# Kernel optimization log

Measured on AMD Instinct MI355X. Metric: run time of the kernel, lower is better.

The kernel has to match this reference:

```python
import jax, jax.numpy as jnp
import numpy as np

EPS = 1e-5
NUM_HEADS = 4


def setup_inputs() -> dict:
    key = jax.random.key(0)
    ks = jax.random.split(key, 6)
    B, C, H, W = 16, 256, 32, 32
    x = jax.random.normal(ks[0], (B, C, H, W), dtype=jnp.float32)
    gamma = jnp.ones((C,), jnp.float32)
    beta = jnp.zeros((C,), jnp.float32)
    run_mean = jax.random.normal(ks[1], (C,), dtype=jnp.float32) * 0.1
    run_var = jax.random.uniform(ks[2], (C,), dtype=jnp.float32, minval=0.5, maxval=1.5)
    qkv_w = jax.random.normal(ks[3], (3 * C, C), dtype=jnp.float32) * (1.0 / np.sqrt(C))
    qkv_b = jnp.zeros((3 * C,), jnp.float32)
    out_w = jax.random.normal(ks[4], (C, C), dtype=jnp.float32) * (1.0 / np.sqrt(C))
    out_b = jnp.zeros((C,), jnp.float32)
    return {"x": x, "gamma": gamma, "beta": beta, "run_mean": run_mean,
            "run_var": run_var, "qkv_w": qkv_w, "qkv_b": qkv_b,
            "out_w": out_w, "out_b": out_b}


def reference(x, gamma, beta, run_mean, run_var, qkv_w, qkv_b, out_w, out_b):
    B, C, H, W = x.shape
    n = NUM_HEADS
    hd = C // n
    # BatchNorm2d (eval mode, running stats)
    inv = jax.lax.rsqrt(run_var + EPS)
    xn = (x - run_mean[:, None, None]) * (inv * gamma)[:, None, None] + beta[:, None, None]
    # 1x1 conv -> QKV: [B, 3C, H, W]
    qkv = jnp.einsum('oc,bchw->bohw', qkv_w, xn) + qkv_b[:, None, None]
    qkv = qkv.reshape(B, n, 3 * hd, H, W)
    q, k, v = qkv[:, :, :hd], qkv[:, :, hd:2 * hd], qkv[:, :, 2 * hd:]
    # full spatial attention; note scale is sqrt(C), per source
    attn = jnp.einsum('bnchw,bncyx->bnhwyx', q, k) / jnp.sqrt(jnp.float32(C))
    attn = jax.nn.softmax(attn.reshape(B, n, H, W, H * W), axis=-1)
    attn = attn.reshape(B, n, H, W, H, W)
    av = jnp.einsum('bnhwyx,bncyx->bnchw', attn, v).reshape(B, C, H, W)
    out = jnp.einsum('oc,bchw->bohw', out_w, av) + out_b[:, None, None]
    return x + out
```

## Files before the change

### kernel.cpp

```cpp
#include <hip/hip_runtime.h>
#include <hip/hip_bf16.h>

__device__ __forceinline__ float bf2f(unsigned short u) {
    return __uint_as_float(((unsigned int)u) << 16);
}
__device__ __forceinline__ unsigned short f2bf(float f) {
    unsigned int u = __float_as_uint(f);
    unsigned int r = (u + 0x7fffu + ((u >> 16) & 1u)) >> 16;
    return (unsigned short)r;
}
__device__ __forceinline__ float ld1(const void* p, long i, bool isf32) {
    return isf32 ? ((const float*)p)[i] : bf2f(((const unsigned short*)p)[i]);
}

typedef __attribute__((ext_vector_type(8))) short bh8;
typedef __attribute__((ext_vector_type(4))) float f32x4;

#define S_TOK 1024
#define C_DIM 256
#define O_QKV 768
#define HD    64
#define NREG  196608
#define QOFF  0
#define KOFF  65536
#define VOFF  131072

__global__ __launch_bounds__(256) void prep_kernel(
    const void* __restrict__ gamma, const void* __restrict__ beta,
    const void* __restrict__ rmean, const void* __restrict__ rvar,
    const void* __restrict__ qkv_w, const void* __restrict__ qkv_b,
    const void* __restrict__ out_w, const void* __restrict__ out_b,
    unsigned short* __restrict__ w1b, float* __restrict__ b1,
    unsigned short* __restrict__ w2b, float* __restrict__ b2, int* __restrict__ flg)
{
    const unsigned g0 = *(const unsigned*)gamma;
    const bool isf32 = (g0 == 0x3F800000u);
    const int c = threadIdx.x;
    const int blk = blockIdx.x;
    if (blk == 0 && c == 0) flg[0] = isf32 ? 1 : 0;
    if (blk < O_QKV) {
        const int o = blk;
        const float v  = ld1(rvar, c, isf32);
        const float a  = ld1(gamma, c, isf32) * rsqrtf(fmaxf(v, 0.f) + 1e-5f);
        const float sh = ld1(beta, c, isf32) - ld1(rmean, c, isf32) * a;
        const float w  = ld1(qkv_w, (long)o * C_DIM + c, isf32);
        w1b[(size_t)o * C_DIM + c] = f2bf(w * a);
        __shared__ float red[256];
        red[c] = w * sh;
        __syncthreads();
        for (int st = 128; st > 0; st >>= 1) {
            if (c < st) red[c] += red[c + st];
            __syncthreads();
        }
        if (c == 0) b1[o] = ld1(qkv_b, o, isf32) + red[0];
    } else {
        const int o = blk - O_QKV;
        w2b[(size_t)o * C_DIM + c] = f2bf(ld1(out_w, (long)o * C_DIM + c, isf32));
        if (c == 0) b2[o] = ld1(out_b, o, isf32);
    }
}

__global__ __launch_bounds__(256) void gemm_qkv_kernel(
    const unsigned short* __restrict__ w1b, const float* __restrict__ b1,
    const void* __restrict__ x, unsigned short* __restrict__ qkv, int b0,
    const int* __restrict__ flg)
{
    const bool isf32 = (flg[0] != 0);
    const int s0 = blockIdx.x * 64;
    const int og = blockIdx.y;
    const int z  = blockIdx.z;
    const int b  = b0 + z;
    const int t  = threadIdx.x;
    const int wave = t >> 6, lane = t & 63;
    const int quad = lane >> 4, l16 = lane & 15;

    __shared__ unsigned short xs[64 * 258];

    const int tok = lane;
#pragma unroll
    for (int it = 0; it < 16; ++it) {
        const int c = (it * 4 + wave) * 4;
        ushort4 w;
        if (isf32) {
            const float* xp = (const float*)x + ((size_t)b * C_DIM + c) * S_TOK + s0 + tok;
            w.x = f2bf(xp[0]);
            w.y = f2bf(xp[S_TOK]);
            w.z = f2bf(xp[2 * S_TOK]);
            w.w = f2bf(xp[3 * S_TOK]);
        } else {
            const unsigned short* xp =
                (const unsigned short*)x + ((size_t)b * C_DIM + c) * S_TOK + s0 + tok;
            w.x = xp[0]; w.y = xp[S_TOK]; w.z = xp[2 * S_TOK]; w.w = xp[3 * S_TOK];
        }
        *(ushort4*)&xs[tok * 258 + c] = w;
    }
    __syncthreads();

    for (int ot = 0; ot < 4; ++ot) {
        const int o0 = og * 256 + ot * 64;
        const int ow = o0 + wave * 16 + l16;
        bh8 af[8];
#pragma unroll
        for (int kc = 0; kc < 8; ++kc)
            af[kc] = *(const bh8*)&w1b[(size_t)ow * C_DIM + kc * 32 + quad * 8];
        f32x4 acc[4];
#pragma unroll
        for (int nt = 0; nt < 4; ++nt) acc[nt] = (f32x4){0.f, 0.f, 0.f, 0.f};
#pragma unroll
        for (int kc = 0; kc < 8; ++kc) {
#pragma unroll
            for (int nt = 0; nt < 4; ++nt) {
                const bh8 bf = *(const bh8*)&xs[(nt * 16 + l16) * 258 + kc * 32 + quad * 8];
                acc[nt] = __builtin_amdgcn_mfma_f32_16x16x32_bf16(af[kc], bf, acc[nt], 0, 0, 0);
            }
        }
        const int n      = o0 / 192;
        const int region = (o0 >> 6) % 3;
        const int och    = wave * 16 + quad * 4;
        float bias_r[4];
#pragma unroll
        for (int r = 0; r < 4; ++r) bias_r[r] = b1[o0 + och + r];
        unsigned short* hb = qkv + (size_t)z * O_QKV * S_TOK + n * NREG;
        if (region < 2) {
            const float sc = (region == 0) ? 0.0625f : 1.0f;
            unsigned short* qb = hb + (region == 0 ? QOFF : KOFF);
#pragma unroll
            for (int nt = 0; nt < 4; ++nt) {
                const int tk = s0 + nt * 16 + l16;
                ushort4 rr;
                rr.x = f2bf((acc[nt][0] + bias_r[0]) * sc);
                rr.y = f2bf((acc[nt][1] + bias_r[1]) * sc);
                rr.z = f2bf((acc[nt][2] + bias_r[2]) * sc);
                rr.w = f2bf((acc[nt][3] + bias_r[3]) * sc);
                *(ushort4*)&qb[(size_t)tk * 64 + och] = rr;
            }
        } else {
            unsigned short* vb = hb + VOFF;
#pragma unroll
            for (int nt = 0; nt < 4; ++nt) {
                const int tk = s0 + nt * 16 + l16;
#pragma unroll
                for (int r = 0; r < 4; ++r)
                    vb[(size_t)(och + r) * S_TOK + tk] = f2bf(acc[nt][r] + bias_r[r]);
            }
        }
    }
}

__global__ __launch_bounds__(256, 4) void attn_mfma_kernel(
    const unsigned short* __restrict__ qkv, unsigned short* __restrict__ av)
{
    const int n  = blockIdx.x & 3;
    const int z  = blockIdx.x >> 2;
    const int qt = blockIdx.y;
    const int q0 = qt * 64;
    const int t  = threadIdx.x;
    const int wave = t >> 6, lane = t & 63;
    const int quad = lane >> 4, l16 = lane & 15;

    const unsigned short* qtp = qkv + (size_t)z * O_QKV * S_TOK + n * NREG + QOFF;
    const unsigned short* ktp = qtp + KOFF;
    const unsigned short* vcp = qtp + VOFF;

    __shared__ unsigned short p_lds[64 * 72];
    __shared__ float rs_lds[64 * 4];

    bh8 qf[4][2];
#pragma unroll
    for (int qs = 0; qs < 4; ++qs) {
        const size_t qrow = (size_t)(q0 + qs * 16 + l16) * 64;
        qf[qs][0] = *(const bh8*)&qtp[qrow + quad * 8];
        qf[qs][1] = *(const bh8*)&qtp[qrow + 32 + quad * 8];
    }

    f32x4 oacc[4];
#pragma unroll
    for (int i = 0; i < 4; ++i) oacc[i] = (f32x4){0.f, 0.f, 0.f, 0.f};
    float rs[4][4];
#pragma unroll
    for (int qs = 0; qs < 4; ++qs)
#pragma unroll
        for (int r = 0; r < 4; ++r) rs[qs][r] = 0.f;

    for (int chunk = 0; chunk < 16; ++chunk) {
        const int c0 = chunk * 64;
        const size_t krow = (size_t)(c0 + wave * 16 + l16) * 64;
        const bh8 kf0 = *(const bh8*)&ktp[krow + quad * 8];
        const bh8 kf1 = *(const bh8*)&ktp[krow + 32 + quad * 8];
        const size_t vrow = (size_t)(wave * 16 + l16) * S_TOK + c0;
        const bh8 vf0 = *(const bh8*)&vcp[vrow + quad * 8];
        const bh8 vf1 = *(const bh8*)&vcp[vrow + 32 + quad * 8];

        f32x4 sacc[4];
#pragma unroll
        for (int qs = 0; qs < 4; ++qs) {
            f32x4 a = (f32x4){0.f, 0.f, 0.f, 0.f};
            a = __builtin_amdgcn_mfma_f32_16x16x32_bf16(qf[qs][0], kf0, a, 0, 0, 0);
            a = __builtin_amdgcn_mfma_f32_16x16x32_bf16(qf[qs][1], kf1, a, 0, 0, 0);
            sacc[qs] = a;
        }
        __syncthreads();
#pragma unroll
        for (int qs = 0; qs < 4; ++qs) {
#pragma unroll
            for (int r = 0; r < 4; ++r) {
                const float p = __expf(sacc[qs][r] - 8.0f);
                rs[qs][r] += p;
                p_lds[(qs * 16 + quad * 4 + r) * 72 + wave * 16 + l16] = f2bf(p);
            }
        }
        __syncthreads();
#pragma unroll
        for (int qs = 0; qs < 4; ++qs) {
            const bh8 pf0 = *(const bh8*)&p_lds[(qs * 16 + l16) * 72 + quad * 8];
            const bh8 pf1 = *(const bh8*)&p_lds[(qs * 16 + l16) * 72 + 32 + quad * 8];
            oacc[qs] = __builtin_amdgcn_mfma_f32_16x16x32_bf16(pf0, vf0, oacc[qs], 0, 0, 0);
            oacc[qs] = __builtin_amdgcn_mfma_f32_16x16x32_bf16(pf1, vf1, oacc[qs], 0, 0, 0);
        }
    }
#pragma unroll
    for (int off = 1; off < 16; off <<= 1) {
#pragma unroll
        for (int qs = 0; qs < 4; ++qs)
#pragma unroll
            for (int r = 0; r < 4; ++r) rs[qs][r] += __shfl_xor(rs[qs][r], off);
    }
    if (l16 == 0) {
#pragma unroll
        for (int qs = 0; qs < 4; ++qs)
#pragma unroll
            for (int r = 0; r < 4; ++r)
                rs_lds[(qs * 16 + quad * 4 + r) * 4 + wave] = rs[qs][r];
    }
    __syncthreads();
    const int ch = n * HD + wave * 16 + l16;
    unsigned short* avb = av + ((size_t)z * C_DIM + ch) * S_TOK + q0;
#pragma unroll
    for (int qs = 0; qs < 4; ++qs) {
        ushort4 st;
        float o[4];
#pragma unroll
        for (int r = 0; r < 4; ++r) {
            const int q = qs * 16 + quad * 4 + r;
            const float4 rw = *(const float4*)&rs_lds[q * 4];
            const float inv = 1.0f / (rw.x + rw.y + rw.z + rw.w);
            o[r] = oacc[qs][r] * inv;
        }
        st.x = f2bf(o[0]); st.y = f2bf(o[1]); st.z = f2bf(o[2]); st.w = f2bf(o[3]);
        *(ushort4*)&avb[qs * 16 + quad * 4] = st;
    }
}

__global__ __launch_bounds__(256) void gemm_out_kernel(
    const unsigned short* __restrict__ w2b, const float* __restrict__ b2,
    const void* __restrict__ x, const unsigned short* __restrict__ av,
    void* __restrict__ out, int b0, const int* __restrict__ flg)
{
    const bool isf32 = (flg[0] != 0);
    const int s0 = blockIdx.x * 64;
    const int og = blockIdx.y;
    const int z  = blockIdx.z;
    const int b  = b0 + z;
    const int t  = threadIdx.x;
    const int wave = t >> 6, lane = t & 63;
    const int quad = lane >> 4, l16 = lane & 15;

    __shared__ unsigned short vs_lds[64 * 258];

    const int tok = lane;
#pragma unroll
    for (int it = 0; it < 16; ++it) {
        const int c = (it * 4 + wave) * 4;
        const unsigned short* ap = av + ((size_t)z * C_DIM + c) * S_TOK + s0 + tok;
        ushort4 w;
        w.x = ap[0]; w.y = ap[S_TOK]; w.z = ap[2 * S_TOK]; w.w = ap[3 * S_TOK];
        *(ushort4*)&vs_lds[tok * 258 + c] = w;
    }
    __syncthreads();

    for (int ot = 0; ot < 2; ++ot) {
        const int o0 = og * 128 + ot * 64;
        const int ow = o0 + wave * 16 + l16;
        bh8 af[8];
#pragma unroll
        for (int kc = 0; kc < 8; ++kc)
            af[kc] = *(const bh8*)&w2b[(size_t)ow * C_DIM + kc * 32 + quad * 8];
        f32x4 acc[4];
#pragma unroll
        for (int nt = 0; nt < 4; ++nt) acc[nt] = (f32x4){0.f, 0.f, 0.f, 0.f};
#pragma unroll
        for (int kc = 0; kc < 8; ++kc) {
#pragma unroll
            for (int nt = 0; nt < 4; ++nt) {
                const bh8 bf = *(const bh8*)&vs_lds[(nt * 16 + l16) * 258 + kc * 32 + quad * 8];
                acc[nt] = __builtin_amdgcn_mfma_f32_16x16x32_bf16(af[kc], bf, acc[nt], 0, 0, 0);
            }
        }
        const int obase = o0 + wave * 16 + quad * 4;
        float bias_r[4];
#pragma unroll
        for (int r = 0; r < 4; ++r) bias_r[r] = b2[obase + r];
#pragma unroll
        for (int nt = 0; nt < 4; ++nt) {
            const int tk = s0 + nt * 16 + l16;
#pragma unroll
            for (int r = 0; r < 4; ++r) {
                const size_t base = ((size_t)b * C_DIM + obase + r) * S_TOK + tk;
                if (isf32) {
                    ((float*)out)[base] = acc[nt][r] + bias_r[r] + ((const float*)x)[base];
                } else {
                    ((unsigned short*)out)[base] =
                        f2bf(acc[nt][r] + bias_r[r] + bf2f(((const unsigned short*)x)[base]));
                }
            }
        }
    }
}

extern "C" void kernel_launch(void* const* d_in, const int* in_sizes, int n_in,
                              void* d_out, int out_size, void* d_ws, size_t ws_size,
                              hipStream_t stream)
{
    const void* x     = d_in[0];
    const void* gamma = d_in[1];
    const void* beta  = d_in[2];
    const void* rmean = d_in[3];
    const void* rvar  = d_in[4];
    const void* qkv_w = d_in[5];
    const void* qkv_b = d_in[6];
    const void* out_w = d_in[7];
    const void* out_b = d_in[8];

    unsigned short* w1b = (unsigned short*)d_ws;
    unsigned short* w2b = w1b + 768 * 256;
    float* b1 = (float*)(w2b + 256 * 256);
    float* b2 = b1 + 768;
    int*   flg = (int*)(b2 + 256);
    const size_t fixed_bytes = (768 * 256 + 256 * 256) * 2 + (768 + 256) * 4 + 16;
    const size_t per_b = (size_t)(768 * 1024 + 256 * 1024) * 2;

    long long avail = (long long)ws_size - (long long)fixed_bytes;
    int G = (avail > 0) ? (int)(avail / (long long)per_b) : 1;
    if (G < 1) G = 1;
    if (G > 16) G = 16;

    unsigned short* qkv = (unsigned short*)((char*)d_ws + fixed_bytes);
    unsigned short* av  = qkv + (size_t)G * 768 * 1024;

    prep_kernel<<<1024, 256, 0, stream>>>(gamma, beta, rmean, rvar, qkv_w, qkv_b,
                                          out_w, out_b, w1b, b1, w2b, b2, flg);
    for (int b0 = 0; b0 < 16; b0 += G) {
        const int gb = (16 - b0 < G) ? (16 - b0) : G;
        gemm_qkv_kernel<<<dim3(16, 3, gb), 256, 0, stream>>>(w1b, b1, x, qkv, b0, flg);
        attn_mfma_kernel<<<dim3(4 * gb, 16, 1), 256, 0, stream>>>(qkv, av);
        gemm_out_kernel<<<dim3(16, 2, gb), 256, 0, stream>>>(w2b, b2, x, av, d_out, b0, flg);
    }
}
```

Baseline: 176.8 us.

## Store activations token-major so GEMMs read MFMA operands directly from global memory

The x transpose to bf16 token-major xT moves into the prep kernel. The attention output is now written token-major through an LDS transpose, so both GEMM kernels drop their strided LDS staging and load MFMA B operands directly from global memory. The GEMM grids are split finer (64 output channels per block) to add parallelism. The P matrix is also converted to bf16 by truncation instead of rounding. The cost is an extra full pass over x in prep, a workspace larger by 8 MB, and redundant global reads of the B tiles across output-channel blocks.

```diff
diff --git a/kernel.cpp b/kernel.cpp
--- a/kernel.cpp
+++ b/kernel.cpp
@@ -30,16 +30,18 @@
     const void* __restrict__ rmean, const void* __restrict__ rvar,
     const void* __restrict__ qkv_w, const void* __restrict__ qkv_b,
     const void* __restrict__ out_w, const void* __restrict__ out_b,
+    const void* __restrict__ x,
     unsigned short* __restrict__ w1b, float* __restrict__ b1,
-    unsigned short* __restrict__ w2b, float* __restrict__ b2, int* __restrict__ flg)
+    unsigned short* __restrict__ w2b, float* __restrict__ b2,
+    unsigned short* __restrict__ xT, int* __restrict__ flg)
 {
     const unsigned g0 = *(const unsigned*)gamma;
     const bool isf32 = (g0 == 0x3F800000u);
-    const int c = threadIdx.x;
+    const int t   = threadIdx.x;
     const int blk = blockIdx.x;
-    if (blk == 0 && c == 0) flg[0] = isf32 ? 1 : 0;
+    if (blk == 0 && t == 0) flg[0] = isf32 ? 1 : 0;
     if (blk < O_QKV) {
-        const int o = blk;
+        const int c = t, o = blk;
         const float v  = ld1(rvar, c, isf32);
         const float a  = ld1(gamma, c, isf32) * rsqrtf(fmaxf(v, 0.f) + 1e-5f);
         const float sh = ld1(beta, c, isf32) - ld1(rmean, c, isf32) * a;
@@ -53,102 +55,99 @@
             __syncthreads();
         }
         if (c == 0) b1[o] = ld1(qkv_b, o, isf32) + red[0];
-    } else {
-        const int o = blk - O_QKV;
+    } else if (blk < 1024) {
+        const int c = t, o = blk - O_QKV;
         w2b[(size_t)o * C_DIM + c] = f2bf(ld1(out_w, (long)o * C_DIM + c, isf32));
         if (c == 0) b2[o] = ld1(out_b, o, isf32);
+    } else {
+        const int idx = blk - 1024;
+        const int b   = idx >> 6;
+        const int s0  = (idx & 15) * 64;
+        const int c0  = ((idx >> 4) & 3) * 64;
+        __shared__ unsigned short ts[64 * 66];
+        const int wave = t >> 6, lane = t & 63;
+#pragma unroll
+        for (int it = 0; it < 16; ++it) {
+            const int ci = it * 4 + wave;
+            const float v = ld1(x, ((size_t)b * C_DIM + c0 + ci) * S_TOK + s0 + lane, isf32);
+            ts[lane * 66 + ci] = f2bf(v);
+        }
+        __syncthreads();
+        const int tok = t >> 2, cq = t & 3;
+        const uint4 a0 = *(const uint4*)&ts[tok * 66 + cq * 16];
+        const uint4 a1 = *(const uint4*)&ts[tok * 66 + cq * 16 + 8];
+        unsigned short* dst = xT + (((size_t)b << 10) + s0 + tok) * C_DIM + c0 + cq * 16;
+        *(uint4*)dst = a0;
+        *(uint4*)(dst + 8) = a1;
     }
 }
 
 __global__ __launch_bounds__(256) void gemm_qkv_kernel(
     const unsigned short* __restrict__ w1b, const float* __restrict__ b1,
-    const void* __restrict__ x, unsigned short* __restrict__ qkv, int b0,
-    const int* __restrict__ flg)
-{
-    const bool isf32 = (flg[0] != 0);
+    const unsigned short* __restrict__ xT, unsigned short* __restrict__ qkv,
+    int b0)
+{
     const int s0 = blockIdx.x * 64;
-    const int og = blockIdx.y;
+    const int o0 = blockIdx.y * 64;
     const int z  = blockIdx.z;
     const int b  = b0 + z;
     const int t  = threadIdx.x;
     const int wave = t >> 6, lane = t & 63;
     const int quad = lane >> 4, l16 = lane & 15;
 
-    __shared__ unsigned short xs[64 * 258];
-
-    const int tok = lane;
-#pragma unroll
-    for (int it = 0; it < 16; ++it) {
-        const int c = (it * 4 + wave) * 4;
-        ushort4 w;
-        if (isf32) {
-            const float* xp = (const float*)x + ((size_t)b * C_DIM + c) * S_TOK + s0 + tok;
-            w.x = f2bf(xp[0]);
-            w.y = f2bf(xp[S_TOK]);
-            w.z = f2bf(xp[2 * S_TOK]);
-            w.w = f2bf(xp[3 * S_TOK]);
-        } else {
-            const unsigned short* xp =
-                (const unsigned short*)x + ((size_t)b * C_DIM + c) * S_TOK + s0 + tok;
-            w.x = xp[0]; w.y = xp[S_TOK]; w.z = xp[2 * S_TOK]; w.w = xp[3 * S_TOK];
-        }
-        *(ushort4*)&xs[tok * 258 + c] = w;
-    }
-    __syncthreads();
-
-    for (int ot = 0; ot < 4; ++ot) {
-        const int o0 = og * 256 + ot * 64;
-        const int ow = o0 + wave * 16 + l16;
-        bh8 af[8];
-#pragma unroll
-        for (int kc = 0; kc < 8; ++kc)
-            af[kc] = *(const bh8*)&w1b[(size_t)ow * C_DIM + kc * 32 + quad * 8];
-        f32x4 acc[4];
-#pragma unroll
-        for (int nt = 0; nt < 4; ++nt) acc[nt] = (f32x4){0.f, 0.f, 0.f, 0.f};
-#pragma unroll
-        for (int kc = 0; kc < 8; ++kc) {
-#pragma unroll
-            for (int nt = 0; nt < 4; ++nt) {
-                const bh8 bf = *(const bh8*)&xs[(nt * 16 + l16) * 258 + kc * 32 + quad * 8];
-                acc[nt] = __builtin_amdgcn_mfma_f32_16x16x32_bf16(af[kc], bf, acc[nt], 0, 0, 0);
-            }
-        }
-        const int n      = o0 / 192;
-        const int region = (o0 >> 6) % 3;
-        const int och    = wave * 16 + quad * 4;
-        float bias_r[4];
-#pragma unroll
-        for (int r = 0; r < 4; ++r) bias_r[r] = b1[o0 + och + r];
-        unsigned short* hb = qkv + (size_t)z * O_QKV * S_TOK + n * NREG;
-        if (region < 2) {
-            const float sc = (region == 0) ? 0.0625f : 1.0f;
-            unsigned short* qb = hb + (region == 0 ? QOFF : KOFF);
-#pragma unroll
-            for (int nt = 0; nt < 4; ++nt) {
-                const int tk = s0 + nt * 16 + l16;
-                ushort4 rr;
-                rr.x = f2bf((acc[nt][0] + bias_r[0]) * sc);
-                rr.y = f2bf((acc[nt][1] + bias_r[1]) * sc);
-                rr.z = f2bf((acc[nt][2] + bias_r[2]) * sc);
-                rr.w = f2bf((acc[nt][3] + bias_r[3]) * sc);
-                *(ushort4*)&qb[(size_t)tk * 64 + och] = rr;
-            }
-        } else {
-            unsigned short* vb = hb + VOFF;
-#pragma unroll
-            for (int nt = 0; nt < 4; ++nt) {
-                const int tk = s0 + nt * 16 + l16;
-#pragma unroll
-                for (int r = 0; r < 4; ++r)
-                    vb[(size_t)(och + r) * S_TOK + tk] = f2bf(acc[nt][r] + bias_r[r]);
-            }
+    const unsigned short* xb = xT + ((size_t)b << 10) * C_DIM;
+    const int ow = o0 + wave * 16 + l16;
+    bh8 af[8];
+#pragma unroll
+    for (int kc = 0; kc < 8; ++kc)
+        af[kc] = *(const bh8*)&w1b[(size_t)ow * C_DIM + kc * 32 + quad * 8];
+
+    f32x4 acc[4];
+#pragma unroll
+    for (int nt = 0; nt < 4; ++nt) acc[nt] = (f32x4){0.f, 0.f, 0.f, 0.f};
+#pragma unroll
+    for (int kc = 0; kc < 8; ++kc) {
+#pragma unroll
+        for (int nt = 0; nt < 4; ++nt) {
+            const bh8 bf = *(const bh8*)&xb[(size_t)(s0 + nt * 16 + l16) * C_DIM +
+                                            kc * 32 + quad * 8];
+            acc[nt] = __builtin_amdgcn_mfma_f32_16x16x32_bf16(af[kc], bf, acc[nt], 0, 0, 0);
+        }
+    }
+    const int n      = o0 / 192;
+    const int region = (o0 >> 6) % 3;
+    const int och    = wave * 16 + quad * 4;
+    float bias_r[4];
+#pragma unroll
+    for (int r = 0; r < 4; ++r) bias_r[r] = b1[o0 + och + r];
+    unsigned short* hb = qkv + (size_t)z * O_QKV * S_TOK + n * NREG;
+    if (region < 2) {
+        const float sc = (region == 0) ? 0.0625f : 1.0f;
+        unsigned short* qb = hb + (region == 0 ? QOFF : KOFF);
+#pragma unroll
+        for (int nt = 0; nt < 4; ++nt) {
+            const int tk = s0 + nt * 16 + l16;
+            ushort4 rr;
+            rr.x = f2bf((acc[nt][0] + bias_r[0]) * sc);
+            rr.y = f2bf((acc[nt][1] + bias_r[1]) * sc);
+            rr.z = f2bf((acc[nt][2] + bias_r[2]) * sc);
+            rr.w = f2bf((acc[nt][3] + bias_r[3]) * sc);
+            *(ushort4*)&qb[(size_t)tk * 64 + och] = rr;
+        }
+    } else {
+        unsigned short* vb = hb + VOFF;
+#pragma unroll
+        for (int nt = 0; nt < 4; ++nt) {
+            const int tk = s0 + nt * 16 + l16;
+#pragma unroll
+            for (int r = 0; r < 4; ++r)
+                vb[(size_t)(och + r) * S_TOK + tk] = f2bf(acc[nt][r] + bias_r[r]);
         }
     }
 }
 
 __global__ __launch_bounds__(256, 4) void attn_mfma_kernel(
-    const unsigned short* __restrict__ qkv, unsigned short* __restrict__ av)
+    const unsigned short* __restrict__ qkv, unsigned short* __restrict__ avT)
 {
     const int n  = blockIdx.x & 3;
     const int z  = blockIdx.x >> 2;
@@ -206,7 +205,8 @@
             for (int r = 0; r < 4; ++r) {
                 const float p = __expf(sacc[qs][r] - 8.0f);
                 rs[qs][r] += p;
-                p_lds[(qs * 16 + quad * 4 + r) * 72 + wave * 16 + l16] = f2bf(p);
+                p_lds[(qs * 16 + quad * 4 + r) * 72 + wave * 16 + l16] =
+                    (unsigned short)(__float_as_uint(p) >> 16);
             }
         }
         __syncthreads();
@@ -233,85 +233,74 @@
                 rs_lds[(qs * 16 + quad * 4 + r) * 4 + wave] = rs[qs][r];
     }
     __syncthreads();
-    const int ch = n * HD + wave * 16 + l16;
-    unsigned short* avb = av + ((size_t)z * C_DIM + ch) * S_TOK + q0;
+    const int ch = wave * 16 + l16;
 #pragma unroll
     for (int qs = 0; qs < 4; ++qs) {
-        ushort4 st;
-        float o[4];
 #pragma unroll
         for (int r = 0; r < 4; ++r) {
             const int q = qs * 16 + quad * 4 + r;
             const float4 rw = *(const float4*)&rs_lds[q * 4];
             const float inv = 1.0f / (rw.x + rw.y + rw.z + rw.w);
-            o[r] = oacc[qs][r] * inv;
-        }
-        st.x = f2bf(o[0]); st.y = f2bf(o[1]); st.z = f2bf(o[2]); st.w = f2bf(o[3]);
-        *(ushort4*)&avb[qs * 16 + quad * 4] = st;
-    }
+            p_lds[q * 72 + ch] = f2bf(oacc[qs][r] * inv);
+        }
+    }
+    __syncthreads();
+    const int tok = t >> 2, cq = t & 3;
+    const uint4 w0 = *(const uint4*)&p_lds[tok * 72 + cq * 16];
+    const uint4 w1 = *(const uint4*)&p_lds[tok * 72 + cq * 16 + 8];
+    unsigned short* dst = avT + (((size_t)z << 10) + q0 + tok) * C_DIM + n * HD + cq * 16;
+    *(uint4*)dst = w0;
+    *(uint4*)(dst + 8) = w1;
 }
 
 __global__ __launch_bounds__(256) void gemm_out_kernel(
     const unsigned short* __restrict__ w2b, const float* __restrict__ b2,
-    const void* __restrict__ x, const unsigned short* __restrict__ av,
+    const void* __restrict__ x, const unsigned short* __restrict__ avT,
     void* __restrict__ out, int b0, const int* __restrict__ flg)
 {
     const bool isf32 = (flg[0] != 0);
     const int s0 = blockIdx.x * 64;
-    const int og = blockIdx.y;
+    const int o0 = blockIdx.y * 64;
     const int z  = blockIdx.z;
     const int b  = b0 + z;
     const int t  = threadIdx.x;
     const int wave = t >> 6, lane = t & 63;
     const int quad = lane >> 4, l16 = lane & 15;
 
-    __shared__ unsigned short vs_lds[64 * 258];
-
-    const int tok = lane;
-#pragma unroll
-    for (int it = 0; it < 16; ++it) {
-        const int c = (it * 4 + wave) * 4;
-        const unsigned short* ap = av + ((size_t)z * C_DIM + c) * S_TOK + s0 + tok;
-        ushort4 w;
-        w.x = ap[0]; w.y = ap[S_TOK]; w.z = ap[2 * S_TOK]; w.w = ap[3 * S_TOK];
-        *(ushort4*)&vs_lds[tok * 258 + c] = w;
-    }
-    __syncthreads();
-
-    for (int ot = 0; ot < 2; ++ot) {
-        const int o0 = og * 128 + ot * 64;
-        const int ow = o0 + wave * 16 + l16;
-        bh8 af[8];
-#pragma unroll
-        for (int kc = 0; kc < 8; ++kc)
-            af[kc] = *(const bh8*)&w2b[(size_t)ow * C_DIM + kc * 32 + quad * 8];
-        f32x4 acc[4];
-#pragma unroll
-        for (int nt = 0; nt < 4; ++nt) acc[nt] = (f32x4){0.f, 0.f, 0.f, 0.f};
-#pragma unroll
-        for (int kc = 0; kc < 8; ++kc) {
-#pragma unroll
-            for (int nt = 0; nt < 4; ++nt) {
-                const bh8 bf = *(const bh8*)&vs_lds[(nt * 16 + l16) * 258 + kc * 32 + quad * 8];
-                acc[nt] = __builtin_amdgcn_mfma_f32_16x16x32_bf16(af[kc], bf, acc[nt], 0, 0, 0);
-            }
-        }
-        const int obase = o0 + wave * 16 + quad * 4;
-        float bias_r[4];
-#pragma unroll
-        for (int r = 0; r < 4; ++r) bias_r[r] = b2[obase + r];
+    const unsigned short* ab = avT + ((size_t)z << 10) * C_DIM;
+    const int ow = o0 + wave * 16 + l16;
+    bh8 af[8];
+#pragma unroll
+    for (int kc = 0; kc < 8; ++kc)
+        af[kc] = *(const bh8*)&w2b[(size_t)ow * C_DIM + kc * 32 + quad * 8];
+
+    f32x4 acc[4];
+#pragma unroll
+    for (int nt = 0; nt < 4; ++nt) acc[nt] = (f32x4){0.f, 0.f, 0.f, 0.f};
+#pragma unroll
+    for (int kc = 0; kc < 8; ++kc) {
 #pragma unroll
         for (int nt = 0; nt < 4; ++nt) {
-            const int tk = s0 + nt * 16 + l16;
-#pragma unroll
-            for (int r = 0; r < 4; ++r) {
-                const size_t base = ((size_t)b * C_DIM + obase + r) * S_TOK + tk;
-                if (isf32) {
-                    ((float*)out)[base] = acc[nt][r] + bias_r[r] + ((const float*)x)[base];
-                } else {
-                    ((unsigned short*)out)[base] =
-                        f2bf(acc[nt][r] + bias_r[r] + bf2f(((const unsigned short*)x)[base]));
-                }
+            const bh8 bf = *(const bh8*)&ab[(size_t)(s0 + nt * 16 + l16) * C_DIM +
+                                            kc * 32 + quad * 8];
+            acc[nt] = __builtin_amdgcn_mfma_f32_16x16x32_bf16(af[kc], bf, acc[nt], 0, 0, 0);
+        }
+    }
+    const int obase = o0 + wave * 16 + quad * 4;
+    float bias_r[4];
+#pragma unroll
+    for (int r = 0; r < 4; ++r) bias_r[r] = b2[obase + r];
+#pragma unroll
+    for (int nt = 0; nt < 4; ++nt) {
+        const int tk = s0 + nt * 16 + l16;
+#pragma unroll
+        for (int r = 0; r < 4; ++r) {
+            const size_t base = ((size_t)b * C_DIM + obase + r) * S_TOK + tk;
+            if (isf32) {
+                ((float*)out)[base] = acc[nt][r] + bias_r[r] + ((const float*)x)[base];
+            } else {
+                ((unsigned short*)out)[base] =
+                    f2bf(acc[nt][r] + bias_r[r] + bf2f(((const unsigned short*)x)[base]));
             }
         }
     }
@@ -336,7 +325,9 @@
     float* b1 = (float*)(w2b + 256 * 256);
     float* b2 = b1 + 768;
     int*   flg = (int*)(b2 + 256);
-    const size_t fixed_bytes = (768 * 256 + 256 * 256) * 2 + (768 + 256) * 4 + 16;
+    unsigned short* xT = (unsigned short*)(flg + 4);
+    const size_t fixed_bytes = (768 * 256 + 256 * 256) * 2 + (768 + 256) * 4 + 16
+                             + (size_t)16 * 1024 * 256 * 2;
     const size_t per_b = (size_t)(768 * 1024 + 256 * 1024) * 2;
 
     long long avail = (long long)ws_size - (long long)fixed_bytes;
@@ -345,14 +336,14 @@
     if (G > 16) G = 16;
 
     unsigned short* qkv = (unsigned short*)((char*)d_ws + fixed_bytes);
-    unsigned short* av  = qkv + (size_t)G * 768 * 1024;
-
-    prep_kernel<<<1024, 256, 0, stream>>>(gamma, beta, rmean, rvar, qkv_w, qkv_b,
-                                          out_w, out_b, w1b, b1, w2b, b2, flg);
+    unsigned short* avT = qkv + (size_t)G * 768 * 1024;
+
+    prep_kernel<<<2048, 256, 0, stream>>>(gamma, beta, rmean, rvar, qkv_w, qkv_b,
+                                          out_w, out_b, x, w1b, b1, w2b, b2, xT, flg);
     for (int b0 = 0; b0 < 16; b0 += G) {
         const int gb = (16 - b0 < G) ? (16 - b0) : G;
-        gemm_qkv_kernel<<<dim3(16, 3, gb), 256, 0, stream>>>(w1b, b1, x, qkv, b0, flg);
-        attn_mfma_kernel<<<dim3(4 * gb, 16, 1), 256, 0, stream>>>(qkv, av);
-        gemm_out_kernel<<<dim3(16, 2, gb), 256, 0, stream>>>(w2b, b2, x, av, d_out, b0, flg);
-    }
-}
+        gemm_qkv_kernel<<<dim3(16, 12, gb), 256, 0, stream>>>(w1b, b1, xT, qkv, b0);
+        attn_mfma_kernel<<<dim3(4 * gb, 16, 1), 256, 0, stream>>>(qkv, avT);
+        gemm_out_kernel<<<dim3(16, 4, gb), 256, 0, stream>>>(w2b, b2, x, avT, d_out, b0, flg);
+    }
+}
```

Result: slower. 209.7 us (+18.6%).
